# Kernel optimization log

Hardware: AMD Instinct MI355X
Metric: run time of the kernel (lower is better)

Reference implementation:

```python
import jax, jax.numpy as jnp
import numpy as np

ITERATIONS = 3

def setup_inputs() -> dict:
    key = jax.random.key(0)
    k1, k2 = jax.random.split(key)
    C, S, H = 64, 128, 2048
    x = jax.random.normal(k1, (C, S, H), dtype=jnp.float32)
    W = jax.random.normal(k2, (H, H), dtype=jnp.float32)
    return {"x": x, "W": W}

def reference(x, W):
    # x: [C, S, H], W: [H, H]
    C, S, H = x.shape
    # e_ij is loop-invariant in the original; hoist it (same math, computed once)
    e_ij = jnp.einsum('csh,hk->csk', x, W)  # [C, S, H]
    b_ij = jnp.zeros((C, S), dtype=x.dtype)
    c_i = jnp.zeros((C, H), dtype=x.dtype)
    for _ in range(ITERATIONS):
        d_i = jax.nn.softmax(b_ij, axis=1)[:, :, None]          # [C, S, 1], softmax over S
        c_i = jnp.sum(d_i * e_ij, axis=1)                        # [C, H]
        squared = jnp.sum(c_i ** 2, axis=1, keepdims=True)       # [C, 1]
        coeff = squared / (1.0 + squared) / jnp.sqrt(squared + 1e-9)
        c_i = coeff * c_i                                        # squash
        b_ij = b_ij + jnp.einsum('csh,ch->cs', e_ij, c_i)        # logit update
    return c_i
```

## Files before the change

### kernel.cpp

```cpp
#include <hip/hip_runtime.h>

using bf16x8 = __attribute__((ext_vector_type(8))) __bf16;
using f32x4  = __attribute__((ext_vector_type(4))) float;

#define C_ 64
#define S_ 128
#define H_ 2048
#define M_ 8192

__device__ __forceinline__ unsigned short f2bf(float f) {
  unsigned u = __float_as_uint(f);
  u = u + 0x7fffu + ((u >> 16) & 1u);
  return (unsigned short)(u >> 16);
}
__device__ __forceinline__ float bf2f(unsigned short h) {
  return __uint_as_float(((unsigned)h) << 16);
}

__device__ __forceinline__ void glds16(const unsigned short* g, unsigned short* l) {
  __builtin_amdgcn_global_load_lds(
      (const __attribute__((address_space(1))) void*)g,
      (__attribute__((address_space(3))) void*)l, 16, 0, 0);
}

__global__ void k_split_all(const float* __restrict__ x,
                            unsigned short* __restrict__ xh,
                            unsigned short* __restrict__ xl,
                            const float* __restrict__ W,
                            unsigned short* __restrict__ Wth,
                            unsigned short* __restrict__ Wtl,
                            float* __restrict__ G) {
  __shared__ float Ts[64][68];
  const int b = blockIdx.x;
  const int t = threadIdx.x;
  if (b < 16384) {
    int idx = b * 256 + t;
    float4 v = ((const float4*)x)[idx];
    float a[4] = {v.x, v.y, v.z, v.w};
    unsigned short h[4], l[4];
#pragma unroll
    for (int q = 0; q < 4; ++q) {
      h[q] = f2bf(a[q]);
      l[q] = f2bf(a[q] - bf2f(h[q]));
    }
    ((ushort4*)xh)[idx] = make_ushort4(h[0], h[1], h[2], h[3]);
    ((ushort4*)xl)[idx] = make_ushort4(l[0], l[1], l[2], l[3]);
  } else if (b < 17408) {
    const int bb = b - 16384;
    const int k0 = (bb & 31) * 64, n0 = (bb >> 5) * 64;
#pragma unroll
    for (int p = 0; p < 4; ++p) {
      int idx = t + p * 256;
      int r = idx >> 4, c4 = (idx & 15) * 4;
      *(float4*)&Ts[r][c4] = *(const float4*)(W + (size_t)(k0 + r) * H_ + n0 + c4);
    }
    __syncthreads();
#pragma unroll
    for (int p = 0; p < 4; ++p) {
      int idx = t + p * 256;
      int rr = idx >> 4, cc = (idx & 15) * 4;
      unsigned short h[4], l[4];
#pragma unroll
      for (int q = 0; q < 4; ++q) {
        float f = Ts[cc + q][rr];
        h[q] = f2bf(f);
        l[q] = f2bf(f - bf2f(h[q]));
      }
      size_t o = (size_t)(n0 + rr) * H_ + k0 + cc;
      *(ushort4*)(Wth + o) = make_ushort4(h[0], h[1], h[2], h[3]);
      *(ushort4*)(Wtl + o) = make_ushort4(l[0], l[1], l[2], l[3]);
    }
  } else {
    const int bb = b - 17408;
    ((float4*)G)[bb * 256 + t] = (float4){0.f, 0.f, 0.f, 0.f};
  }
}

__global__ __launch_bounds__(256, 4) void k_gemm3(
    const unsigned short* __restrict__ Ah, const unsigned short* __restrict__ Al,
    const unsigned short* __restrict__ Bh, const unsigned short* __restrict__ Bl,
    unsigned short* __restrict__ Eh, unsigned short* __restrict__ El) {
  __shared__ unsigned short sAh[128 * 32], sAl[128 * 32], sBh[128 * 32], sBl[128 * 32];
  const int t = threadIdx.x;
  const int bm = blockIdx.x, bn = blockIdx.y;
  const int lane = t & 63, wid = t >> 6;
  const int wm = wid >> 1, wn = wid & 1;
  const int l16 = lane & 15, quad = lane >> 4;

  const int rl = lane >> 2;
  const int gg = (lane & 3) ^ ((rl >> 1) & 3);
  const int c0 = wid * 2, c1 = wid * 2 + 1;
  const unsigned short* gAh0 = Ah + (size_t)(bm * 128 + c0 * 16 + rl) * H_ + gg * 8;
  const unsigned short* gAh1 = Ah + (size_t)(bm * 128 + c1 * 16 + rl) * H_ + gg * 8;
  const unsigned short* gAl0 = Al + (size_t)(bm * 128 + c0 * 16 + rl) * H_ + gg * 8;
  const unsigned short* gAl1 = Al + (size_t)(bm * 128 + c1 * 16 + rl) * H_ + gg * 8;
  const unsigned short* gBh0 = Bh + (size_t)(bn * 128 + c0 * 16 + rl) * H_ + gg * 8;
  const unsigned short* gBh1 = Bh + (size_t)(bn * 128 + c1 * 16 + rl) * H_ + gg * 8;
  const unsigned short* gBl0 = Bl + (size_t)(bn * 128 + c0 * 16 + rl) * H_ + gg * 8;
  const unsigned short* gBl1 = Bl + (size_t)(bn * 128 + c1 * 16 + rl) * H_ + gg * 8;
  unsigned short* lA0 = sAh + c0 * 512;
  unsigned short* lA1 = sAh + c1 * 512;
  unsigned short* lAl0 = sAl + c0 * 512;
  unsigned short* lAl1 = sAl + c1 * 512;
  unsigned short* lB0 = sBh + c0 * 512;
  unsigned short* lB1 = sBh + c1 * 512;
  unsigned short* lBl0 = sBl + c0 * 512;
  unsigned short* lBl1 = sBl + c1 * 512;

  const int swz = ((l16 >> 1) & 3);
  const int colq = ((quad ^ swz) * 8);

  f32x4 acc[4][4];
#pragma unroll
  for (int i = 0; i < 4; ++i)
#pragma unroll
    for (int j = 0; j < 4; ++j) acc[i][j] = (f32x4)0.f;

  for (int k0 = 0; k0 < H_; k0 += 32) {
    __syncthreads();
    glds16(gAh0 + k0, lA0);
    glds16(gAh1 + k0, lA1);
    glds16(gAl0 + k0, lAl0);
    glds16(gAl1 + k0, lAl1);
    glds16(gBh0 + k0, lB0);
    glds16(gBh1 + k0, lB1);
    glds16(gBl0 + k0, lBl0);
    glds16(gBl1 + k0, lBl1);
    __syncthreads();

    bf16x8 ah[4], al[4], bh[4], bl[4];
#pragma unroll
    for (int i = 0; i < 4; ++i) {
      const int ra = (wm * 64 + i * 16 + l16) * 32;
      const int rb = (wn * 64 + i * 16 + l16) * 32;
      ah[i] = *(const bf16x8*)&sAh[ra + colq];
      al[i] = *(const bf16x8*)&sAl[ra + colq];
      bh[i] = *(const bf16x8*)&sBh[rb + colq];
      bl[i] = *(const bf16x8*)&sBl[rb + colq];
    }
#pragma unroll
    for (int i = 0; i < 4; ++i)
#pragma unroll
      for (int j = 0; j < 4; ++j) {
        acc[i][j] = __builtin_amdgcn_mfma_f32_16x16x32_bf16(ah[i], bh[j], acc[i][j], 0, 0, 0);
        acc[i][j] = __builtin_amdgcn_mfma_f32_16x16x32_bf16(ah[i], bl[j], acc[i][j], 0, 0, 0);
        acc[i][j] = __builtin_amdgcn_mfma_f32_16x16x32_bf16(al[i], bh[j], acc[i][j], 0, 0, 0);
      }
  }

#pragma unroll
  for (int i = 0; i < 4; ++i) {
    const int row0 = bm * 128 + wm * 64 + i * 16 + quad * 4;
#pragma unroll
    for (int j = 0; j < 4; ++j) {
      const int col = bn * 128 + wn * 64 + j * 16 + l16;
#pragma unroll
      for (int r = 0; r < 4; ++r) {
        float v = acc[i][j][r];
        unsigned short hh = f2bf(v);
        unsigned short ll = f2bf(v - bf2f(hh));
        Eh[(size_t)(row0 + r) * H_ + col] = hh;
        El[(size_t)(row0 + r) * H_ + col] = ll;
      }
    }
  }
}

__global__ __launch_bounds__(256, 4) void k_gram_mfma(
    const unsigned short* __restrict__ Eh, const unsigned short* __restrict__ El,
    float* __restrict__ G) {
  __shared__ unsigned short sH[128 * 32], sL[128 * 32];
  const int t = threadIdx.x;
  const int kc = blockIdx.x;
  const int cc = blockIdx.y;
  const int lane = t & 63, wid = t >> 6;
  const int wm = wid >> 1, wn = wid & 1;
  const int l16 = lane & 15, quad = lane >> 4;

  const int rl = lane >> 2;
  const int gg = (lane & 3) ^ ((rl >> 1) & 3);
  const int c0 = wid * 2, c1 = c0 + 1;
  const unsigned short* gH0 = Eh + (size_t)(cc * 128 + c0 * 16 + rl) * H_ + gg * 8;
  const unsigned short* gH1 = Eh + (size_t)(cc * 128 + c1 * 16 + rl) * H_ + gg * 8;
  const unsigned short* gL0 = El + (size_t)(cc * 128 + c0 * 16 + rl) * H_ + gg * 8;
  const unsigned short* gL1 = El + (size_t)(cc * 128 + c1 * 16 + rl) * H_ + gg * 8;
  unsigned short* lH0 = sH + c0 * 512;
  unsigned short* lH1 = sH + c1 * 512;
  unsigned short* lL0 = sL + c0 * 512;
  unsigned short* lL1 = sL + c1 * 512;

  const int swz = ((l16 >> 1) & 3);
  const int colq = ((quad ^ swz) * 8);

  f32x4 acc[4][4];
#pragma unroll
  for (int i = 0; i < 4; ++i)
#pragma unroll
    for (int j = 0; j < 4; ++j) acc[i][j] = (f32x4)0.f;

  const int kbeg = kc * 512;
  for (int k0 = kbeg; k0 < kbeg + 512; k0 += 32) {
    __syncthreads();
    glds16(gH0 + k0, lH0);
    glds16(gH1 + k0, lH1);
    glds16(gL0 + k0, lL0);
    glds16(gL1 + k0, lL1);
    __syncthreads();

    bf16x8 ah[4], al[4], bh[4], bl[4];
#pragma unroll
    for (int i = 0; i < 4; ++i) {
      const int ra = (wm * 64 + i * 16 + l16) * 32;
      const int rb = (wn * 64 + i * 16 + l16) * 32;
      ah[i] = *(const bf16x8*)&sH[ra + colq];
      al[i] = *(const bf16x8*)&sL[ra + colq];
      bh[i] = *(const bf16x8*)&sH[rb + colq];
      bl[i] = *(const bf16x8*)&sL[rb + colq];
    }
#pragma unroll
    for (int i = 0; i < 4; ++i)
#pragma unroll
      for (int j = 0; j < 4; ++j) {
        acc[i][j] = __builtin_amdgcn_mfma_f32_16x16x32_bf16(ah[i], bh[j], acc[i][j], 0, 0, 0);
        acc[i][j] = __builtin_amdgcn_mfma_f32_16x16x32_bf16(ah[i], bl[j], acc[i][j], 0, 0, 0);
        acc[i][j] = __builtin_amdgcn_mfma_f32_16x16x32_bf16(al[i], bh[j], acc[i][j], 0, 0, 0);
      }
  }

  float* Gc = G + (size_t)cc * S_ * S_;
#pragma unroll
  for (int i = 0; i < 4; ++i) {
    const int row0 = wm * 64 + i * 16 + quad * 4;
#pragma unroll
    for (int j = 0; j < 4; ++j) {
      const int col = wn * 64 + j * 16 + l16;
#pragma unroll
      for (int r = 0; r < 4; ++r)
        atomicAdd(&Gc[(row0 + r) * S_ + col], acc[i][j][r]);
    }
  }
}

__global__ void k_out2(const unsigned short* __restrict__ Eh,
                       const unsigned short* __restrict__ El,
                       const float* __restrict__ G, float* __restrict__ out) {
  const int c = blockIdx.y;
  const int s = threadIdx.x & 127;
  __shared__ float dsh[128];
  __shared__ float red[128];
  __shared__ float wsh[128];
  const float* Gc = G + (size_t)c * S_ * S_;
  float b = 0.f;
  for (int it = 0; it < 3; ++it) {
    red[s] = b; __syncthreads();
    for (int off = 64; off > 0; off >>= 1) {
      if (s < off) red[s] = fmaxf(red[s], red[s + off]);
      __syncthreads();
    }
    float mx = red[0]; __syncthreads();
    float ev = expf(b - mx);
    red[s] = ev; __syncthreads();
    for (int off = 64; off > 0; off >>= 1) {
      if (s < off) red[s] = red[s] + red[s + off];
      __syncthreads();
    }
    float Z = red[0]; __syncthreads();
    float d = ev / Z;
    dsh[s] = d; __syncthreads();
    float y = 0.f;
#pragma unroll 8
    for (int j = 0; j < S_; ++j) y = fmaf(Gc[j * S_ + s], dsh[j], y);
    red[s] = d * y; __syncthreads();
    for (int off = 64; off > 0; off >>= 1) {
      if (s < off) red[s] = red[s] + red[s + off];
      __syncthreads();
    }
    float sq = red[0]; __syncthreads();
    float coeff = sq / (1.f + sq) / sqrtf(sq + 1e-9f);
    if (it == 2) wsh[s] = coeff * d;
    else b += coeff * y;
  }
  __syncthreads();

  const int h2 = blockIdx.x * 256 + threadIdx.x;
  const unsigned* Ph = (const unsigned*)(Eh + (size_t)c * S_ * H_) + h2;
  const unsigned* Pl = (const unsigned*)(El + (size_t)c * S_ * H_) + h2;
  float a0 = 0.f, a1 = 0.f;
#pragma unroll 8
  for (int ss = 0; ss < S_; ++ss) {
    unsigned uh = Ph[(size_t)ss * (H_ / 2)];
    unsigned ul = Pl[(size_t)ss * (H_ / 2)];
    a0 = fmaf(wsh[ss], bf2f((unsigned short)uh) + bf2f((unsigned short)ul), a0);
    a1 = fmaf(wsh[ss], bf2f((unsigned short)(uh >> 16)) + bf2f((unsigned short)(ul >> 16)), a1);
  }
  ((float2*)(out + (size_t)c * H_))[h2] = make_float2(a0, a1);
}

extern "C" void kernel_launch(void* const* d_in, const int* in_sizes, int n_in,
                              void* d_out, int out_size, void* d_ws, size_t ws_size,
                              hipStream_t stream) {
  (void)in_sizes; (void)n_in; (void)out_size; (void)ws_size;
  const float* x = (const float*)d_in[0];
  const float* W = (const float*)d_in[1];
  float* out = (float*)d_out;
  char* ws = (char*)d_ws;

  unsigned short* xh  = (unsigned short*)(ws);
  unsigned short* xl  = (unsigned short*)(ws + 33554432);
  unsigned short* Wth = (unsigned short*)(ws + 67108864);
  unsigned short* Wtl = (unsigned short*)(ws + 75497472);
  unsigned short* Eh  = (unsigned short*)(ws + 83886080);
  unsigned short* El  = (unsigned short*)(ws + 117440512);
  float*          G   = (float*)(ws + 150994944);

  k_split_all<<<dim3(18432), 256, 0, stream>>>(x, xh, xl, W, Wth, Wtl, G);
  k_gemm3<<<dim3(64, 16), 256, 0, stream>>>(xh, xl, Wth, Wtl, Eh, El);
  k_gram_mfma<<<dim3(4, 64), 256, 0, stream>>>(Eh, El, G);
  k_out2<<<dim3(4, 64), 256, 0, stream>>>(Eh, El, G, out);
}
```

Before: 372.6 us.

## Triple-buffer GEMM with 256x128 tiles, 512 threads, and XCD-aware block mapping

Rewrites the split-bf16 GEMM to use 8 waves per block on a 256x128 output tile. The LDS is a three-stage ring buffer, and the global-to-LDS loads for future K tiles are interleaved between the two halves of the MFMA work, with setprio raising priority during the MFMA sections. Block indices are remapped so neighbouring tiles land on the same XCD to improve L2 reuse. The goal is to hide memory latency and cut sync stalls, at the cost of more LDS (about 147KB) and lower occupancy.

```diff
diff --git a/kernel.cpp b/kernel.cpp
--- a/kernel.cpp
+++ b/kernel.cpp
@@ -76,39 +76,42 @@
   }
 }
 
-__global__ __launch_bounds__(256, 4) void k_gemm3(
+#define TILE_USH 24576
+#define OFF_AH 0
+#define OFF_AL 8192
+#define OFF_BH 16384
+#define OFF_BL 20480
+
+__global__ __launch_bounds__(512, 2) void k_gemm3(
     const unsigned short* __restrict__ Ah, const unsigned short* __restrict__ Al,
     const unsigned short* __restrict__ Bh, const unsigned short* __restrict__ Bl,
     unsigned short* __restrict__ Eh, unsigned short* __restrict__ El) {
-  __shared__ unsigned short sAh[128 * 32], sAl[128 * 32], sBh[128 * 32], sBl[128 * 32];
+  __shared__ unsigned short lds[3 * TILE_USH];
   const int t = threadIdx.x;
-  const int bm = blockIdx.x, bn = blockIdx.y;
   const int lane = t & 63, wid = t >> 6;
   const int wm = wid >> 1, wn = wid & 1;
   const int l16 = lane & 15, quad = lane >> 4;
 
+  const int lin = blockIdx.x + (blockIdx.y << 5);
+  const int xcd = lin & 7, slot = lin >> 3;
+  const int bm = ((xcd >> 1) << 3) + (slot >> 3);
+  const int bn = ((xcd & 1) << 3) + (slot & 7);
+
   const int rl = lane >> 2;
-  const int gg = (lane & 3) ^ ((rl >> 1) & 3);
-  const int c0 = wid * 2, c1 = wid * 2 + 1;
-  const unsigned short* gAh0 = Ah + (size_t)(bm * 128 + c0 * 16 + rl) * H_ + gg * 8;
-  const unsigned short* gAh1 = Ah + (size_t)(bm * 128 + c1 * 16 + rl) * H_ + gg * 8;
-  const unsigned short* gAl0 = Al + (size_t)(bm * 128 + c0 * 16 + rl) * H_ + gg * 8;
-  const unsigned short* gAl1 = Al + (size_t)(bm * 128 + c1 * 16 + rl) * H_ + gg * 8;
-  const unsigned short* gBh0 = Bh + (size_t)(bn * 128 + c0 * 16 + rl) * H_ + gg * 8;
-  const unsigned short* gBh1 = Bh + (size_t)(bn * 128 + c1 * 16 + rl) * H_ + gg * 8;
-  const unsigned short* gBl0 = Bl + (size_t)(bn * 128 + c0 * 16 + rl) * H_ + gg * 8;
-  const unsigned short* gBl1 = Bl + (size_t)(bn * 128 + c1 * 16 + rl) * H_ + gg * 8;
-  unsigned short* lA0 = sAh + c0 * 512;
-  unsigned short* lA1 = sAh + c1 * 512;
-  unsigned short* lAl0 = sAl + c0 * 512;
-  unsigned short* lAl1 = sAl + c1 * 512;
-  unsigned short* lB0 = sBh + c0 * 512;
-  unsigned short* lB1 = sBh + c1 * 512;
-  unsigned short* lBl0 = sBl + c0 * 512;
-  unsigned short* lBl1 = sBl + c1 * 512;
-
-  const int swz = ((l16 >> 1) & 3);
-  const int colq = ((quad ^ swz) * 8);
+  const int gg8 = (((lane & 3) ^ ((rl >> 1) & 3)) << 3);
+  const unsigned short* gAh0 = Ah + (size_t)(bm * 256 + wid * 16 + rl) * H_ + gg8;
+  const unsigned short* gAl0 = Al + (size_t)(bm * 256 + wid * 16 + rl) * H_ + gg8;
+  const unsigned short* gAh1 = gAh0 + (size_t)128 * H_;
+  const unsigned short* gAl1 = gAl0 + (size_t)128 * H_;
+  const unsigned short* gBh  = Bh + (size_t)(bn * 128 + wid * 16 + rl) * H_ + gg8;
+  const unsigned short* gBl  = Bl + (size_t)(bn * 128 + wid * 16 + rl) * H_ + gg8;
+  const int dA0 = wid * 512;
+  const int dA1 = dA0 + 4096;
+  const int dB  = wid * 512;
+
+  const int colq = ((quad ^ ((l16 >> 1) & 3)) << 3);
+  const int rA = (wm * 64 + l16) * 32 + colq;
+  const int rB = (wn * 64 + l16) * 32 + colq;
 
   f32x4 acc[4][4];
 #pragma unroll
@@ -116,41 +119,93 @@
 #pragma unroll
     for (int j = 0; j < 4; ++j) acc[i][j] = (f32x4)0.f;
 
-  for (int k0 = 0; k0 < H_; k0 += 32) {
-    __syncthreads();
-    glds16(gAh0 + k0, lA0);
-    glds16(gAh1 + k0, lA1);
-    glds16(gAl0 + k0, lAl0);
-    glds16(gAl1 + k0, lAl1);
-    glds16(gBh0 + k0, lB0);
-    glds16(gBh1 + k0, lB1);
-    glds16(gBl0 + k0, lBl0);
-    glds16(gBl1 + k0, lBl1);
-    __syncthreads();
-
+  auto stage6 = [&](int bo, int k) {
+    glds16(gAh0 + k, &lds[bo + OFF_AH + dA0]);
+    glds16(gAh1 + k, &lds[bo + OFF_AH + dA1]);
+    glds16(gAl0 + k, &lds[bo + OFF_AL + dA0]);
+    glds16(gAl1 + k, &lds[bo + OFF_AL + dA1]);
+    glds16(gBh + k,  &lds[bo + OFF_BH + dB]);
+    glds16(gBl + k,  &lds[bo + OFF_BL + dB]);
+  };
+
+  auto body = [&](int co, int n2o, int k2, bool issue) {
     bf16x8 ah[4], al[4], bh[4], bl[4];
+    if (issue) {
+      glds16(gAh0 + k2, &lds[n2o + OFF_AH + dA0]);
+      glds16(gAl0 + k2, &lds[n2o + OFF_AL + dA0]);
+      glds16(gBh + k2,  &lds[n2o + OFF_BH + dB]);
+    }
 #pragma unroll
     for (int i = 0; i < 4; ++i) {
-      const int ra = (wm * 64 + i * 16 + l16) * 32;
-      const int rb = (wn * 64 + i * 16 + l16) * 32;
-      ah[i] = *(const bf16x8*)&sAh[ra + colq];
-      al[i] = *(const bf16x8*)&sAl[ra + colq];
-      bh[i] = *(const bf16x8*)&sBh[rb + colq];
-      bl[i] = *(const bf16x8*)&sBl[rb + colq];
-    }
+      ah[i] = *(const bf16x8*)&lds[co + OFF_AH + rA + i * 512];
+      al[i] = *(const bf16x8*)&lds[co + OFF_AL + rA + i * 512];
+    }
+#pragma unroll
+    for (int j = 0; j < 2; ++j) {
+      bh[j] = *(const bf16x8*)&lds[co + OFF_BH + rB + j * 512];
+      bl[j] = *(const bf16x8*)&lds[co + OFF_BL + rB + j * 512];
+    }
+    __builtin_amdgcn_s_barrier();
+    asm volatile("s_waitcnt lgkmcnt(0)" ::: "memory");
+    __builtin_amdgcn_sched_barrier(0);
+    __builtin_amdgcn_s_setprio(1);
 #pragma unroll
     for (int i = 0; i < 4; ++i)
 #pragma unroll
-      for (int j = 0; j < 4; ++j) {
+      for (int j = 0; j < 2; ++j) {
         acc[i][j] = __builtin_amdgcn_mfma_f32_16x16x32_bf16(ah[i], bh[j], acc[i][j], 0, 0, 0);
         acc[i][j] = __builtin_amdgcn_mfma_f32_16x16x32_bf16(ah[i], bl[j], acc[i][j], 0, 0, 0);
         acc[i][j] = __builtin_amdgcn_mfma_f32_16x16x32_bf16(al[i], bh[j], acc[i][j], 0, 0, 0);
       }
-  }
+    __builtin_amdgcn_s_setprio(0);
+    __builtin_amdgcn_s_barrier();
+    if (issue) {
+      glds16(gAh1 + k2, &lds[n2o + OFF_AH + dA1]);
+      glds16(gAl1 + k2, &lds[n2o + OFF_AL + dA1]);
+      glds16(gBl + k2,  &lds[n2o + OFF_BL + dB]);
+    }
+#pragma unroll
+    for (int j = 2; j < 4; ++j) {
+      bh[j] = *(const bf16x8*)&lds[co + OFF_BH + rB + j * 512];
+      bl[j] = *(const bf16x8*)&lds[co + OFF_BL + rB + j * 512];
+    }
+    __builtin_amdgcn_s_barrier();
+    asm volatile("s_waitcnt lgkmcnt(0)" ::: "memory");
+    __builtin_amdgcn_sched_barrier(0);
+    __builtin_amdgcn_s_setprio(1);
+#pragma unroll
+    for (int i = 0; i < 4; ++i)
+#pragma unroll
+      for (int j = 2; j < 4; ++j) {
+        acc[i][j] = __builtin_amdgcn_mfma_f32_16x16x32_bf16(ah[i], bh[j], acc[i][j], 0, 0, 0);
+        acc[i][j] = __builtin_amdgcn_mfma_f32_16x16x32_bf16(ah[i], bl[j], acc[i][j], 0, 0, 0);
+        acc[i][j] = __builtin_amdgcn_mfma_f32_16x16x32_bf16(al[i], bh[j], acc[i][j], 0, 0, 0);
+      }
+    __builtin_amdgcn_s_setprio(0);
+    if (issue) asm volatile("s_waitcnt vmcnt(6)" ::: "memory");
+    else       asm volatile("s_waitcnt vmcnt(0)" ::: "memory");
+    __builtin_amdgcn_s_barrier();
+  };
+
+  stage6(0, 0);
+  stage6(TILE_USH, 32);
+  asm volatile("s_waitcnt vmcnt(6)" ::: "memory");
+  __builtin_amdgcn_s_barrier();
+
+  int cur = 0;
+#pragma unroll 1
+  for (int tt = 0; tt < 62; ++tt) {
+    int n2 = cur + 2; if (n2 >= 3) n2 -= 3;
+    body(cur * TILE_USH, n2 * TILE_USH, (tt + 2) * 32, true);
+    cur = (cur == 2) ? 0 : cur + 1;
+  }
+  body(cur * TILE_USH, 0, 0, false);
+  cur = (cur == 2) ? 0 : cur + 1;
+  body(cur * TILE_USH, 0, 0, false);
 
 #pragma unroll
   for (int i = 0; i < 4; ++i) {
-    const int row0 = bm * 128 + wm * 64 + i * 16 + quad * 4;
+    const int row0 = bm * 256 + wm * 64 + i * 16 + quad * 4;
 #pragma unroll
     for (int j = 0; j < 4; ++j) {
       const int col = bn * 128 + wn * 64 + j * 16 + l16;
@@ -314,7 +369,7 @@
   float*          G   = (float*)(ws + 150994944);
 
   k_split_all<<<dim3(18432), 256, 0, stream>>>(x, xh, xl, W, Wth, Wtl, G);
-  k_gemm3<<<dim3(64, 16), 256, 0, stream>>>(xh, xl, Wth, Wtl, Eh, El);
+  k_gemm3<<<dim3(32, 16), 512, 0, stream>>>(xh, xl, Wth, Wtl, Eh, El);
   k_gram_mfma<<<dim3(4, 64), 256, 0, stream>>>(Eh, El, G);
   k_out2<<<dim3(4, 64), 256, 0, stream>>>(Eh, El, G, out);
 }
```

New measurement: 347.4 us. -6.8%, faster.
